# Kernel optimization log

Measured on AMD Instinct MI355X. Metric: run time of the kernel, lower is better.

Reference implementation:

```python
import jax, jax.numpy as jnp
import numpy as np

# ResNet-20 (CIFAR) conv shapes: conv1 + 18 block convs, all 3x3 pad=1
SHAPES = [(16,3,3,3)] + [(16,16,3,3)]*6 + [(32,16,3,3)] + [(32,32,3,3)]*5 + [(64,32,3,3)] + [(64,64,3,3)]*5
SIZES = [int(np.prod(s)) for s in SHAPES]
OFFS = np.concatenate([[0], np.cumsum(SIZES)]).astype(int)
D = int(OFFS[-1])  # 267696 flattened conv params
LOW_D = 40
# (conv_a, conv_b, stride, out_channels) for each BasicBlock
BLOCKS = [(1,2,1,16),(3,4,1,16),(5,6,1,16),
          (7,8,2,32),(9,10,1,32),(11,12,1,32),
          (13,14,2,64),(15,16,1,64),(17,18,1,64)]

def conv3x3(x, w, stride):
    return jax.lax.conv_general_dilated(x, w, (stride, stride), ((1,1),(1,1)),
        dimension_numbers=('NCHW','OIHW','NCHW'))

def bn(x):
    # training-mode BatchNorm2d with default-initialized affine (gamma=1, beta=0)
    m = jnp.mean(x, axis=(0,2,3), keepdims=True)
    v = jnp.var(x, axis=(0,2,3), keepdims=True)
    return (x - m) * jax.lax.rsqrt(v + 1e-5)

def shortcut(x, stride, out_ch):
    # option-A shortcut: stride-2 subsample + zero-pad channels
    if stride != 1:
        x = x[:, :, ::2, ::2]
    pad = out_ch - x.shape[1]
    if pad > 0:
        x = jnp.pad(x, ((0,0),(pad//2, pad - pad//2),(0,0),(0,0)))
    return x

def setup_inputs() -> dict:
    key = jax.random.key(0)
    ks = jax.random.split(key, 6)
    B = 1024
    x = jax.random.normal(ks[0], (B,3,32,32), jnp.float32)
    origin_weight = jax.random.normal(ks[1], (D,), jnp.float32) * 0.05
    P = jax.random.normal(ks[2], (LOW_D, D), jnp.float32) * 0.01
    new_param = jax.random.uniform(ks[3], (LOW_D,), jnp.float32)
    W_fc = jax.random.normal(ks[4], (10,64), jnp.float32) * 0.1
    b_fc = jnp.zeros((10,), jnp.float32)
    return {"x": x, "origin_weight": origin_weight, "P": P,
            "new_param": new_param, "W_fc": W_fc, "b_fc": b_fc}

def reference(x, origin_weight, P, new_param, W_fc, b_fc):
    # conv(x, W0) + sum_i a_i * conv(x, P_i)  ==  conv(x, W0 + sum_i a_i * P_i)
    # (conv is linear in its weights, so fusing the 40-term loop is exact)
    w_flat = origin_weight + new_param @ P  # [D]
    ws = [w_flat[OFFS[i]:OFFS[i+1]].reshape(SHAPES[i]) for i in range(19)]
    out = jax.nn.relu(bn(conv3x3(x, ws[0], 1)))
    for (a, b, s, c) in BLOCKS:
        h = jax.nn.relu(bn(conv3x3(out, ws[a], s)))
        h = bn(conv3x3(h, ws[b], 1))
        out = jax.nn.relu(h + shortcut(out, s, c))
    out = out.mean(axis=(2,3))  # global average pool -> [B, 64]
    return out @ W_fc.T + b_fc  # [B, 10]
```

## Files before the change

kernel.cpp:

```cpp
#include <hip/hip_runtime.h>
#include <hip/hip_bf16.h>

#define BATCH 1024
#define NLAYER 19
#define DTOT 267696
#define NSLOT 64
#define PSL (NSLOT*128)

typedef __attribute__((ext_vector_type(8))) short v8s;
typedef __attribute__((ext_vector_type(4))) float v4f;

__device__ inline float ldf(const float* p){ return *p; }
__device__ inline float ldf(const __hip_bfloat16* p){ return __bfloat162float(*p); }

__device__ inline unsigned short f2bf(float x){
    __hip_bfloat16 h = __float2bfloat16(x);
    return *reinterpret_cast<unsigned short*>(&h);
}
__device__ inline float bf2f(unsigned int u){
    return __uint_as_float(u << 16);
}

__global__ void detect_kernel(const unsigned short* __restrict__ xraw, int* __restrict__ flag)
{
    __shared__ int bad;
    if (threadIdx.x == 0) bad = 0;
    __syncthreads();
    int lbad = 0;
    for (int i = threadIdx.x; i < 4096; i += 256) {
        unsigned e = (xraw[i] >> 7) & 0xFF;
        if (e >= 147) lbad++;
    }
    if (lbad) atomicAdd(&bad, lbad);
    __syncthreads();
    if (threadIdx.x == 0) *flag = (bad == 0) ? 1 : 0;
}

__device__ inline bool flag_skip(const int* flag, int want)
{
    if (flag == nullptr) return false;
    return (*(volatile const int*)flag) != want;
}

template<typename T>
__global__ void wflat_kernel(const T* __restrict__ origin,
                             const T* __restrict__ P,
                             const T* __restrict__ npar,
                             float* __restrict__ wout, int D,
                             const int* flag, int want)
{
    if (flag_skip(flag, want)) return;
    int d = blockIdx.x*256 + threadIdx.x;
    if (d >= D) return;
    float acc = ldf(origin + d);
    #pragma unroll 8
    for (int k = 0; k < 40; k++)
        acc += ldf(npar + k) * ldf(P + (long long)k*D + d);
    wout[d] = acc;
}

__global__ void wprep_kernel(const float* __restrict__ wflat, unsigned short* __restrict__ WT)
{
    static const int CINA[19]  = {3,16,16,16,16,16,16,16,32,32,32,32,32,32,64,64,64,64,64};
    static const int COUTA[19] = {16,16,16,16,16,16,16,32,32,32,32,32,32,64,64,64,64,64,64};
    static const int LGCA[19]  = {0,4,4,4,4,4,4,4,5,5,5,5,5,5,6,6,6,6,6};
    static const int KPADA[19] = {0,160,160,160,160,160,160,160,288,288,288,288,288,288,576,576,576,576,576};
    static const int WOFFA[19] = {0,432,2736,5040,7344,9648,11952,14256,18864,
        28080,37296,46512,55728,64944,83376,120240,157104,193968,230832};
    static const int WTOFFA[19]= {0,0,2560,5120,7680,10240,12800,15360,20480,29696,
        38912,48128,57344,66560,84992,121856,158720,195584,232448};
    int l = blockIdx.z;
    if (l == 0) return;
    int co = blockIdx.y;
    if (co >= COUTA[l]) return;
    int kp = blockIdx.x*192 + threadIdx.x;
    if (kp >= KPADA[l]) return;
    int cin = CINA[l];
    float v = 0.f;
    if (kp < 9*cin) {
        int tap = kp >> LGCA[l];
        int ci  = kp & (cin - 1);
        v = wflat[WOFFA[l] + (co*cin + ci)*9 + tap];
    }
    WT[WTOFFA[l] + co*KPADA[l] + kp] = f2bf(v);
}

__device__ inline void ldpair(const float* base, int p, float& x0, float& x1){
    const float2 v = ((const float2*)base)[p];
    x0 = v.x; x1 = v.y;
}
__device__ inline void ldpair(const __hip_bfloat16* base, int p, float& x0, float& x1){
    unsigned u = ((const unsigned int*)base)[p];
    x0 = __uint_as_float(u << 16);
    x1 = __uint_as_float(u & 0xffff0000u);
}

template<typename T>
__global__ __launch_bounds__(512) void conv_l0(
    const T* __restrict__ in, const float* __restrict__ wt,
    unsigned short* __restrict__ out,
    const int* flag, int want)
{
    if (flag_skip(flag, want)) return;
    constexpr int WP = 38, W2 = 19;
    __shared__ uint2 smem2[2048];
    __shared__ unsigned int in_su[3*18*W2];

    const int tid  = threadIdx.x;
    const int b    = blockIdx.x >> 1;
    const int half = blockIdx.x & 1;
    const int row0 = half*16 - 1;

    {
        const T* inb = in + (size_t)b*3072;
        for (int i = tid; i < 864; i += 512) {
            int w2 = i & 15, lr = (i >> 4) % 18, c = i / 288;
            int ih = row0 + lr;
            unsigned int pk = 0u;
            if ((unsigned)ih < 32u) {
                float x0, x1;
                ldpair(inb, (c*32 + ih)*16 + w2, x0, x1);
                pk = (unsigned int)f2bf(x0) | ((unsigned int)f2bf(x1) << 16);
            }
            in_su[(c*18 + lr)*W2 + 1 + w2] = pk;
        }
        unsigned short* in_ss = (unsigned short*)in_su;
        for (int i = tid; i < 54; i += 512) {
            in_ss[i*WP + 1]  = 0;
            in_ss[i*WP + 34] = 0;
        }
    }
    __syncthreads();

    const int r   = tid >> 5;
    const int col = tid & 31;
    const bool odd = (col & 1);

    float xin[27];
    #pragma unroll
    for (int ci = 0; ci < 3; ci++) {
        #pragma unroll
        for (int kh = 0; kh < 3; kh++) {
            const unsigned int* up = in_su + (ci*18 + r + kh)*W2 + ((col+1) >> 1);
            unsigned int u0 = up[0], u1 = up[1];
            const int kb = ci*9 + kh*3;
            xin[kb+0] = odd ? bf2f(u0 & 0xffffu) : bf2f(u0 >> 16);
            xin[kb+1] = odd ? bf2f(u0 >> 16)     : bf2f(u1 & 0xffffu);
            xin[kb+2] = odd ? bf2f(u1 & 0xffffu) : bf2f(u1 >> 16);
        }
    }

    float acc[16];
    #pragma unroll
    for (int co = 0; co < 16; co++) {
        float a = 0.f;
        #pragma unroll
        for (int k = 0; k < 27; k++)
            a += xin[k] * wt[co*27 + k];
        acc[co] = a;
    }

    #pragma unroll
    for (int j = 0; j < 4; j++) {
        uint2 v;
        v.x = (unsigned)f2bf(acc[4*j+0]) | ((unsigned)f2bf(acc[4*j+1]) << 16);
        v.y = (unsigned)f2bf(acc[4*j+2]) | ((unsigned)f2bf(acc[4*j+3]) << 16);
        smem2[tid*4 + (j ^ (tid & 3))] = v;
    }
    __syncthreads();
    {
        uint2* ob = (uint2*)(out + (size_t)b*16384 + half*8192);
        #pragma unroll
        for (int it = 0; it < 4; it++) {
            int s = it*512 + tid;
            int phys = (s & ~3) | ((s & 3) ^ ((s >> 2) & 3));
            ob[s] = smem2[phys];
        }
    }
}

__global__ __launch_bounds__(256) void stats16_kernel(
    const unsigned short* __restrict__ x, float* __restrict__ ps, int n4)
{
    __shared__ float red[4][32];
    int t = blockIdx.x*256 + threadIdx.x;
    const int stride = gridDim.x*256;
    float s[4] = {0,0,0,0}, q[4] = {0,0,0,0};
    for (int i = t; i < n4; i += stride) {
        uint2 v = ((const uint2*)x)[i];
        float f0 = bf2f(v.x & 0xffffu), f1 = bf2f(v.x >> 16);
        float f2_ = bf2f(v.y & 0xffffu), f3 = bf2f(v.y >> 16);
        s[0] += f0; q[0] += f0*f0;
        s[1] += f1; q[1] += f1*f1;
        s[2] += f2_; q[2] += f2_*f2_;
        s[3] += f3; q[3] += f3*f3;
    }
    #pragma unroll
    for (int off = 4; off < 64; off <<= 1) {
        #pragma unroll
        for (int k = 0; k < 4; k++) {
            s[k] += __shfl_xor(s[k], off);
            q[k] += __shfl_xor(q[k], off);
        }
    }
    const int lane = threadIdx.x & 63, w = threadIdx.x >> 6;
    if (lane < 4) {
        #pragma unroll
        for (int k = 0; k < 4; k++) {
            red[w][lane*4 + k]      = s[k];
            red[w][16 + lane*4 + k] = q[k];
        }
    }
    __syncthreads();
    if (threadIdx.x < 32) {
        float v = red[0][threadIdx.x] + red[1][threadIdx.x]
                + red[2][threadIdx.x] + red[3][threadIdx.x];
        float* sl = ps + (blockIdx.x & (NSLOT-1))*128;
        atomicAdd(&sl[(threadIdx.x < 16) ? threadIdx.x : (48 + threadIdx.x)], v);
    }
}

template<int CIN, int COUT, int HIN, int WIN, int ST, bool FUSE, bool PN,
         bool FUSE2, int PREVC, int PADF>
__global__ __launch_bounds__(256, 4) void conv_mfma(
    const unsigned short* __restrict__ src, const unsigned short* __restrict__ prev,
    unsigned short* __restrict__ resid,
    const unsigned short* __restrict__ wt,
    unsigned short* __restrict__ out, float* __restrict__ stats,
    const float* __restrict__ nstats, float ninvN,
    const float* __restrict__ pstats, float pinvN)
{
    constexpr int HO = HIN/ST, WO = WIN/ST, M = HO*WO, MT = M/16;
    constexpr int NT = COUT/16;
    constexpr int K  = 9*CIN;
    constexpr int S  = (K + 31)/32;
    constexpr int KPAD = S*32;
    constexpr int lgC  = (CIN==16)?4:(CIN==32)?5:6;
    constexpr int lgWI = (WIN==32)?5:(WIN==16)?4:3;
    constexpr int lgWO = (WO==32)?5:(WO==16)?4:3;
    constexpr int CMASK = CIN/8 - 1;
    constexpr int JITER = (NT==1)? MT/4 : (NT==2)? MT/2 : MT;
    static_assert(M*COUT <= CIN*HIN*WIN, "out_s fits in in_s");

    __shared__ unsigned short in_s[CIN*HIN*WIN];
    __shared__ float red[128];
    __shared__ float statred[256];
    __shared__ float nm[64], nv[64];
    __shared__ float pm_s[64], pv_s[64];
    __shared__ uint4 zq;

    const int tid = threadIdx.x;
    const int b   = blockIdx.x;

    if (tid == 0) { zq.x = 0; zq.y = 0; zq.z = 0; zq.w = 0; }

    if (nstats != nullptr) {
        const int idx = tid & 127, hf = tid >> 7;
        float sacc = 0.f;
        #pragma unroll 8
        for (int k = hf*32; k < hf*32 + 32; k++)
            sacc += nstats[k*128 + idx];
        statred[tid] = sacc;
    }
    __syncthreads();
    if (nstats != nullptr && tid < CIN) {
        float ssum = statred[tid]      + statred[128 + tid];
        float qsum = statred[64 + tid] + statred[192 + tid];
        float m = ssum*ninvN;
        float v = fmaxf(qsum*ninvN - m*m, 0.f);
        nm[tid] = m; nv[tid] = rsqrtf(v + 1e-5f);
    }
    if (PN && tid < CIN) {
        float ssum = 0.f, qsum = 0.f;
        for (int k = 0; k < NSLOT; k++) {
            ssum += pstats[k*128 + tid];
            qsum += pstats[k*128 + 64 + tid];
        }
        float m = ssum*pinvN;
        float v = fmaxf(qsum*pinvN - m*m, 0.f);
        pm_s[tid] = m; pv_s[tid] = rsqrtf(v + 1e-5f);
    }
    __syncthreads();

    {
        const uint4* sb4 = (const uint4*)(src + (size_t)b*(HIN*WIN)*CIN);
        constexpr int NP4 = CIN*HIN*WIN/8;
        if (FUSE) {
            const uint4* pb4 = (const uint4*)(prev + (size_t)b*(HIN*WIN)*CIN);
            uint4* rb4 = (uint4*)(resid + (size_t)b*(HIN*WIN)*CIN);
            for (int i = tid; i < NP4; i += 256) {
                uint4 v = sb4[i];
                uint4 pw = pb4[i];
                int e0 = i << 3;
                int c0 = e0 & (CIN-1);
                int p  = e0 >> lgC;
                float f[8] = { bf2f(v.x & 0xffffu), bf2f(v.x >> 16),
                               bf2f(v.y & 0xffffu), bf2f(v.y >> 16),
                               bf2f(v.z & 0xffffu), bf2f(v.z >> 16),
                               bf2f(v.w & 0xffffu), bf2f(v.w >> 16) };
                float g[8] = { bf2f(pw.x & 0xffffu), bf2f(pw.x >> 16),
                               bf2f(pw.y & 0xffffu), bf2f(pw.y >> 16),
                               bf2f(pw.z & 0xffffu), bf2f(pw.z >> 16),
                               bf2f(pw.w & 0xffffu), bf2f(pw.w >> 16) };
                #pragma unroll
                for (int k = 0; k < 8; k++) {
                    int c = c0 + k;
                    float fx = (f[k] - nm[c])*nv[c];
                    float gv = g[k];
                    if (PN) gv = fmaxf((gv - pm_s[c])*pv_s[c], 0.f);
                    f[k] = fmaxf(fx + gv, 0.f);
                }
                uint4 o;
                o.x = (unsigned)f2bf(f[0]) | ((unsigned)f2bf(f[1]) << 16);
                o.y = (unsigned)f2bf(f[2]) | ((unsigned)f2bf(f[3]) << 16);
                o.z = (unsigned)f2bf(f[4]) | ((unsigned)f2bf(f[5]) << 16);
                o.w = (unsigned)f2bf(f[6]) | ((unsigned)f2bf(f[7]) << 16);
                rb4[i] = o;
                int csw = c0 ^ ((p & CMASK) << 3);
                *(uint4*)(in_s + (p << lgC) + csw) = o;
            }
        } else if (FUSE2) {
            uint4* rb4 = (uint4*)(resid + (size_t)b*(HIN*WIN)*CIN);
            for (int i = tid; i < NP4; i += 256) {
                uint4 v = sb4[i];
                int e0 = i << 3;
                int c0 = e0 & (CIN-1);
                int p  = e0 >> lgC;
                int h  = p >> lgWI, wq = p & (WIN-1);
                int pp = (h << (lgWI+2)) + 2*wq;
                int pc0 = c0 - PADF;
                bool pv = (pc0 >= 0) && (pc0 <= PREVC - 8);
                uint4 pw;
                pw.x = 0; pw.y = 0; pw.z = 0; pw.w = 0;
                if (pv) pw = *(const uint4*)(prev + ((size_t)b*(HIN*WIN*4) + pp)*PREVC + pc0);
                float f[8] = { bf2f(v.x & 0xffffu), bf2f(v.x >> 16),
                               bf2f(v.y & 0xffffu), bf2f(v.y >> 16),
                               bf2f(v.z & 0xffffu), bf2f(v.z >> 16),
                               bf2f(v.w & 0xffffu), bf2f(v.w >> 16) };
                float g[8] = { bf2f(pw.x & 0xffffu), bf2f(pw.x >> 16),
                               bf2f(pw.y & 0xffffu), bf2f(pw.y >> 16),
                               bf2f(pw.z & 0xffffu), bf2f(pw.z >> 16),
                               bf2f(pw.w & 0xffffu), bf2f(pw.w >> 16) };
                #pragma unroll
                for (int k = 0; k < 8; k++) {
                    int c = c0 + k;
                    f[k] = fmaxf((f[k] - nm[c])*nv[c] + g[k], 0.f);
                }
                uint4 o;
                o.x = (unsigned)f2bf(f[0]) | ((unsigned)f2bf(f[1]) << 16);
                o.y = (unsigned)f2bf(f[2]) | ((unsigned)f2bf(f[3]) << 16);
                o.z = (unsigned)f2bf(f[4]) | ((unsigned)f2bf(f[5]) << 16);
                o.w = (unsigned)f2bf(f[6]) | ((unsigned)f2bf(f[7]) << 16);
                rb4[i] = o;
                int csw = c0 ^ ((p & CMASK) << 3);
                *(uint4*)(in_s + (p << lgC) + csw) = o;
            }
        } else if (nstats == nullptr) {
            for (int i = tid; i < NP4; i += 256) {
                uint4 v = sb4[i];
                int e0 = i << 3;
                int c0 = e0 & (CIN-1);
                int p  = e0 >> lgC;
                int csw = c0 ^ ((p & CMASK) << 3);
                *(uint4*)(in_s + (p << lgC) + csw) = v;
            }
        } else {
            for (int i = tid; i < NP4; i += 256) {
                uint4 v = sb4[i];
                int e0 = i << 3;
                int c0 = e0 & (CIN-1);
                int p  = e0 >> lgC;
                float f[8] = { bf2f(v.x & 0xffffu), bf2f(v.x >> 16),
                               bf2f(v.y & 0xffffu), bf2f(v.y >> 16),
                               bf2f(v.z & 0xffffu), bf2f(v.z >> 16),
                               bf2f(v.w & 0xffffu), bf2f(v.w >> 16) };
                #pragma unroll
                for (int k = 0; k < 8; k++) {
                    int c = c0 + k;
                    f[k] = fmaxf((f[k] - nm[c])*nv[c], 0.f);
                }
                uint4 o;
                o.x = (unsigned)f2bf(f[0]) | ((unsigned)f2bf(f[1]) << 16);
                o.y = (unsigned)f2bf(f[2]) | ((unsigned)f2bf(f[3]) << 16);
                o.z = (unsigned)f2bf(f[4]) | ((unsigned)f2bf(f[5]) << 16);
                o.w = (unsigned)f2bf(f[6]) | ((unsigned)f2bf(f[7]) << 16);
                int csw = c0 ^ ((p & CMASK) << 3);
                *(uint4*)(in_s + (p << lgC) + csw) = o;
            }
        }
    }
    __syncthreads();

    const int w   = tid >> 6;
    const int ln  = tid & 63;
    const int l15 = ln & 15;
    const int q   = ln >> 4;

    int n0, mt0, step;
    if (NT == 1)      { n0 = 0;         mt0 = w;      step = 4; }
    else if (NT == 2) { n0 = (w&1)*16;  mt0 = w>>1;   step = 2; }
    else              { n0 = w*16;      mt0 = 0;      step = 1; }

    v8s Bf[S];
    {
        const unsigned short* wb = wt + (size_t)(n0 + l15)*KPAD + q*8;
        #pragma unroll
        for (int s = 0; s < S; s++)
            Bf[s] = *(const v8s*)(wb + 32*s);
    }

    int dh1s[S], dw1s[S];
    int c0q = (CIN==16) ? ((q & 1) << 3) : (q << 3);
    if (CIN == 16) {
        int tq = q >> 1;
        #pragma unroll
        for (int s = 0; s < S; s++) {
            int tap = 2*s + tq;
            int dh = (tap*11) >> 5;
            int dw = tap - 3*dh;
            dh1s[s] = (tap >= 9) ? -1000 : (dh - 1);
            dw1s[s] = dw - 1;
        }
    }

    v4f acc[JITER];
    #pragma unroll
    for (int j = 0; j < JITER; j++) acc[j] = v4f{0.f,0.f,0.f,0.f};

    #pragma unroll
    for (int j = 0; j < JITER; j++) {
        const int mt  = mt0 + j*step;
        const int p   = mt*16 + l15;
        const int ihb = (p >> lgWO) * ST;
        const int iwb = (p & (WO-1)) * ST;
        #pragma unroll
        for (int s = 0; s < S; s++) {
            int dh1, dw1, c0s;
            if (CIN == 16) { dh1 = dh1s[s]; dw1 = dw1s[s]; c0s = c0q; }
            else {
                const int tap = (CIN == 32) ? s : (s >> 1);
                dh1 = tap/3 - 1; dw1 = tap%3 - 1;
                c0s = c0q + ((CIN == 64) ? ((s & 1) << 5) : 0);
            }
            int ih = ihb + dh1, iw = iwb + dw1;
            bool valid = ((unsigned)ih < (unsigned)HIN) && ((unsigned)iw < (unsigned)WIN);
            int pp  = (ih << lgWI) + iw;
            int csw = c0s ^ ((pp & CMASK) << 3);
            int eoff = (pp << lgC) + csw;
            const v8s* ap = valid ? (const v8s*)(in_s + eoff) : (const v8s*)&zq;
            v8s Af = *ap;
            acc[j] = __builtin_amdgcn_mfma_f32_16x16x32_bf16(Af, Bf[s], acc[j], 0, 0, 0);
        }
    }
    __syncthreads();

    unsigned short* out_s = in_s;
    float sa = 0.f, qa = 0.f;
    #pragma unroll
    for (int j = 0; j < JITER; j++) {
        const int mt = mt0 + j*step;
        #pragma unroll
        for (int r2 = 0; r2 < 4; r2++) {
            float v = acc[j][r2];
            out_s[(mt*16 + q*4 + r2)*COUT + n0 + l15] = f2bf(v);
            sa += v; qa += v*v;
        }
    }
    __syncthreads();

    {
        constexpr int NIT = (M*COUT/8)/256;
        uint4* ob4 = (uint4*)(out + (size_t)b*M*COUT);
        const uint4* os4 = (const uint4*)in_s;
        #pragma unroll
        for (int it = 0; it < NIT; it++)
            ob4[it*256 + tid] = os4[it*256 + tid];
    }

    sa += __shfl_xor(sa, 16); sa += __shfl_xor(sa, 32);
    qa += __shfl_xor(qa, 16); qa += __shfl_xor(qa, 32);
    if (q == 0) {
        red[(w*16 + l15)*2]     = sa;
        red[(w*16 + l15)*2 + 1] = qa;
    }
    __syncthreads();
    if (tid < COUT) {
        float S2, Q2;
        if (NT == 1) {
            S2 = red[tid*2] + red[(16+tid)*2] + red[(32+tid)*2] + red[(48+tid)*2];
            Q2 = red[tid*2+1] + red[(16+tid)*2+1] + red[(32+tid)*2+1] + red[(48+tid)*2+1];
        } else if (NT == 2) {
            int w0 = tid >> 4, cl = tid & 15;
            S2 = red[((w0*16)+cl)*2]     + red[(((w0+2)*16)+cl)*2];
            Q2 = red[((w0*16)+cl)*2 + 1] + red[(((w0+2)*16)+cl)*2 + 1];
        } else {
            int w0 = tid >> 4, cl = tid & 15;
            S2 = red[((w0*16)+cl)*2];
            Q2 = red[((w0*16)+cl)*2 + 1];
        }
        float* sl = stats + (b & (NSLOT-1))*128;
        atomicAdd(&sl[tid],      S2);
        atomicAdd(&sl[64 + tid], Q2);
    }
}

__device__ inline void stf(float* p, float v){ *p = v; }
__device__ inline void stf(__hip_bfloat16* p, float v){ *p = __float2bfloat16(v); }

template<typename T>
__global__ void poolfc_kernel(const unsigned short* __restrict__ x,
    const unsigned short* __restrict__ resid,
    const float* __restrict__ stats, float invN,
    const T* __restrict__ Wfc, const T* __restrict__ bfc,
    T* __restrict__ out, const int* flag, int want)
{
    if (flag_skip(flag, want)) return;
    int b = blockIdx.x;
    int c = threadIdx.x;
    float ssum = 0.f, qsum = 0.f;
    for (int k = 0; k < NSLOT; k++) {
        ssum += stats[k*128 + c];
        qsum += stats[k*128 + 64 + c];
    }
    float m = ssum*invN;
    float v = fmaxf(qsum*invN - m*m, 0.f);
    float rs = rsqrtf(v + 1e-5f);
    float s = 0.f;
    #pragma unroll
    for (int p = 0; p < 64; p++) {
        size_t idx = ((size_t)b*64 + p)*64 + c;
        float xv = bf2f((unsigned int)x[idx]);
        float rv = bf2f((unsigned int)resid[idx]);
        s += fmaxf((xv - m)*rs + rv, 0.f);
    }
    __shared__ float feat[64];
    feat[c] = s * (1.f/64.f);
    __syncthreads();
    if (c < 10) {
        float o = ldf(bfc + c);
        for (int k = 0; k < 64; k++)
            o += feat[k] * ldf(Wfc + c*64 + k);
        stf(out + b*10 + c, o);
    }
}

extern "C" void kernel_launch(void* const* d_in, const int* in_sizes, int n_in,
                              void* d_out, int out_size, void* d_ws, size_t ws_size,
                              hipStream_t stream)
{
    char* ws = (char*)d_ws;
    float* wflat = (float*)(ws);
    int*   flag  = (int*)  (ws + 1146880);
    unsigned short* WT = (unsigned short*)(ws + 1179648);
    unsigned short* curA = (unsigned short*)(ws + 1720320);
    unsigned short* curB = (unsigned short*)(ws + 1720320 + 33554432ULL);
    unsigned short* f1   = (unsigned short*)(ws + 1720320 + 67108864ULL);
    unsigned short* f2   = (unsigned short*)(ws + 1720320 + 100663296ULL);
    float* ps    = (float*)(ws + 135938048ULL);

    hipMemsetAsync(ps, 0, NLAYER*PSL*4, stream);
    detect_kernel<<<1, 256, 0, stream>>>((const unsigned short*)d_in[0], flag);

    wflat_kernel<__hip_bfloat16><<<(DTOT+255)/256, 256, 0, stream>>>(
        (const __hip_bfloat16*)d_in[1], (const __hip_bfloat16*)d_in[2],
        (const __hip_bfloat16*)d_in[3], wflat, DTOT, flag, 1);
    wflat_kernel<float><<<(DTOT+255)/256, 256, 0, stream>>>(
        (const float*)d_in[1], (const float*)d_in[2],
        (const float*)d_in[3], wflat, DTOT, flag, 0);

    {
        dim3 g(3, 64, 19);
        wprep_kernel<<<g, 192, 0, stream>>>(wflat, WT);
    }

    static const int WTOFF[NLAYER] = {0,0,2560,5120,7680,10240,12800,15360,20480,29696,
        38912,48128,57344,66560,84992,121856,158720,195584,232448};
    const float iN32 = 1.f/1048576.f;
    const float iN16 = 1.f/262144.f;
    const float iN8  = 1.f/65536.f;

    conv_l0<__hip_bfloat16><<<2*BATCH,512,0,stream>>>(
        (const __hip_bfloat16*)d_in[0], wflat, curB, flag, 1);
    conv_l0<float><<<2*BATCH,512,0,stream>>>(
        (const float*)d_in[0], wflat, curB, flag, 0);
    stats16_kernel<<<512,256,0,stream>>>(curB, ps, 4194304);

    conv_mfma<16,16,32,32,1,false,false,false,0,0><<<BATCH,256,0,stream>>>(
        curB, nullptr, nullptr, WT + WTOFF[1], f1, ps + 1*PSL, ps, iN32, nullptr, 0.f);
    conv_mfma<16,16,32,32,1,false,false,false,0,0><<<BATCH,256,0,stream>>>(
        f1, nullptr, nullptr, WT + WTOFF[2], f2, ps + 2*PSL, ps + 1*PSL, iN32, nullptr, 0.f);
    conv_mfma<16,16,32,32,1,true,true,false,0,0><<<BATCH,256,0,stream>>>(
        f2, curB, curA, WT + WTOFF[3], f1, ps + 3*PSL, ps + 2*PSL, iN32, ps, iN32);
    conv_mfma<16,16,32,32,1,false,false,false,0,0><<<BATCH,256,0,stream>>>(
        f1, nullptr, nullptr, WT + WTOFF[4], f2, ps + 4*PSL, ps + 3*PSL, iN32, nullptr, 0.f);
    conv_mfma<16,16,32,32,1,true,false,false,0,0><<<BATCH,256,0,stream>>>(
        f2, curA, curB, WT + WTOFF[5], f1, ps + 5*PSL, ps + 4*PSL, iN32, nullptr, 0.f);
    conv_mfma<16,16,32,32,1,false,false,false,0,0><<<BATCH,256,0,stream>>>(
        f1, nullptr, nullptr, WT + WTOFF[6], f2, ps + 6*PSL, ps + 5*PSL, iN32, nullptr, 0.f);
    conv_mfma<16,32,32,32,2,true,false,false,0,0><<<BATCH,256,0,stream>>>(
        f2, curB, curA, WT + WTOFF[7], f1, ps + 7*PSL, ps + 6*PSL, iN32, nullptr, 0.f);
    conv_mfma<32,32,16,16,1,false,false,false,0,0><<<BATCH,256,0,stream>>>(
        f1, nullptr, nullptr, WT + WTOFF[8], f2, ps + 8*PSL, ps + 7*PSL, iN16, nullptr, 0.f);
    conv_mfma<32,32,16,16,1,false,false,true,16,8><<<BATCH,256,0,stream>>>(
        f2, curA, curB, WT + WTOFF[9], f1, ps + 9*PSL, ps + 8*PSL, iN16, nullptr, 0.f);
    conv_mfma<32,32,16,16,1,false,false,false,0,0><<<BATCH,256,0,stream>>>(
        f1, nullptr, nullptr, WT + WTOFF[10], f2, ps + 10*PSL, ps + 9*PSL, iN16, nullptr, 0.f);
    conv_mfma<32,32,16,16,1,true,false,false,0,0><<<BATCH,256,0,stream>>>(
        f2, curB, curA, WT + WTOFF[11], f1, ps + 11*PSL, ps + 10*PSL, iN16, nullptr, 0.f);
    conv_mfma<32,32,16,16,1,false,false,false,0,0><<<BATCH,256,0,stream>>>(
        f1, nullptr, nullptr, WT + WTOFF[12], f2, ps + 12*PSL, ps + 11*PSL, iN16, nullptr, 0.f);
    conv_mfma<32,64,16,16,2,true,false,false,0,0><<<BATCH,256,0,stream>>>(
        f2, curA, curB, WT + WTOFF[13], f1, ps + 13*PSL, ps + 12*PSL, iN16, nullptr, 0.f);
    conv_mfma<64,64,8,8,1,false,false,false,0,0><<<BATCH,256,0,stream>>>(
        f1, nullptr, nullptr, WT + WTOFF[14], f2, ps + 14*PSL, ps + 13*PSL, iN8, nullptr, 0.f);
    conv_mfma<64,64,8,8,1,false,false,true,32,16><<<BATCH,256,0,stream>>>(
        f2, curB, curA, WT + WTOFF[15], f1, ps + 15*PSL, ps + 14*PSL, iN8, nullptr, 0.f);
    conv_mfma<64,64,8,8,1,false,false,false,0,0><<<BATCH,256,0,stream>>>(
        f1, nullptr, nullptr, WT + WTOFF[16], f2, ps + 16*PSL, ps + 15*PSL, iN8, nullptr, 0.f);
    conv_mfma<64,64,8,8,1,true,false,false,0,0><<<BATCH,256,0,stream>>>(
        f2, curA, curB, WT + WTOFF[17], f1, ps + 17*PSL, ps + 16*PSL, iN8, nullptr, 0.f);
    conv_mfma<64,64,8,8,1,false,false,false,0,0><<<BATCH,256,0,stream>>>(
        f1, nullptr, nullptr, WT + WTOFF[18], f2, ps + 18*PSL, ps + 17*PSL, iN8, nullptr, 0.f);

    poolfc_kernel<__hip_bfloat16><<<BATCH, 64, 0, stream>>>(
        f2, curB, ps + 18*PSL, iN8,
        (const __hip_bfloat16*)d_in[4], (const __hip_bfloat16*)d_in[5],
        (__hip_bfloat16*)d_out, flag, 1);
    poolfc_kernel<float><<<BATCH, 64, 0, stream>>>(
        f2, curB, ps + 18*PSL, iN8,
        (const float*)d_in[4], (const float*)d_in[5],
        (float*)d_out, flag, 0);
}
```

Baseline: 471.5 us.

## Fuse layer-0 batchnorm statistics into conv_l0 and stream weights for CIN=64

The per-channel sum and sum-of-squares for the first conv output are now accumulated inside conv_l0 as it writes its tile, which removes the separate stats16_kernel pass that re-read the full activation tensor. For CIN=64 layers the MFMA loop order is swapped so each weight fragment is loaded inside the tap loop instead of holding all S fragments in registers. The aim is lower register pressure and better occupancy, at the cost of repeated weight loads from global/L1. The fused stats path adds 2048 atomics per launch into the same 64 slots.

Measured after the change: 459.2 us. 1.03x faster.

```diff
diff --git a/kernel.cpp b/kernel.cpp
--- a/kernel.cpp
+++ b/kernel.cpp
@@ -98,13 +98,14 @@
 template<typename T>
 __global__ __launch_bounds__(512) void conv_l0(
     const T* __restrict__ in, const float* __restrict__ wt,
-    unsigned short* __restrict__ out,
+    unsigned short* __restrict__ out, float* __restrict__ ps,
     const int* flag, int want)
 {
     if (flag_skip(flag, want)) return;
     constexpr int WP = 38, W2 = 19;
     __shared__ uint2 smem2[2048];
     __shared__ unsigned int in_su[3*18*W2];
+    __shared__ float sred[8][32];
 
     const int tid  = threadIdx.x;
     const int b    = blockIdx.x >> 1;
@@ -168,55 +169,49 @@
         smem2[tid*4 + (j ^ (tid & 3))] = v;
     }
     __syncthreads();
+
+    float s4[4] = {0,0,0,0}, q4[4] = {0,0,0,0};
     {
         uint2* ob = (uint2*)(out + (size_t)b*16384 + half*8192);
         #pragma unroll
         for (int it = 0; it < 4; it++) {
             int s = it*512 + tid;
             int phys = (s & ~3) | ((s & 3) ^ ((s >> 2) & 3));
-            ob[s] = smem2[phys];
-        }
-    }
-}
-
-__global__ __launch_bounds__(256) void stats16_kernel(
-    const unsigned short* __restrict__ x, float* __restrict__ ps, int n4)
-{
-    __shared__ float red[4][32];
-    int t = blockIdx.x*256 + threadIdx.x;
-    const int stride = gridDim.x*256;
-    float s[4] = {0,0,0,0}, q[4] = {0,0,0,0};
-    for (int i = t; i < n4; i += stride) {
-        uint2 v = ((const uint2*)x)[i];
-        float f0 = bf2f(v.x & 0xffffu), f1 = bf2f(v.x >> 16);
-        float f2_ = bf2f(v.y & 0xffffu), f3 = bf2f(v.y >> 16);
-        s[0] += f0; q[0] += f0*f0;
-        s[1] += f1; q[1] += f1*f1;
-        s[2] += f2_; q[2] += f2_*f2_;
-        s[3] += f3; q[3] += f3*f3;
+            uint2 v = smem2[phys];
+            ob[s] = v;
+            float f0 = bf2f(v.x & 0xffffu), f1v = bf2f(v.x >> 16);
+            float f2v = bf2f(v.y & 0xffffu), f3v = bf2f(v.y >> 16);
+            s4[0] += f0;  q4[0] += f0*f0;
+            s4[1] += f1v; q4[1] += f1v*f1v;
+            s4[2] += f2v; q4[2] += f2v*f2v;
+            s4[3] += f3v; q4[3] += f3v*f3v;
+        }
     }
     #pragma unroll
     for (int off = 4; off < 64; off <<= 1) {
         #pragma unroll
-        for (int k = 0; k < 4; k++) {
-            s[k] += __shfl_xor(s[k], off);
-            q[k] += __shfl_xor(q[k], off);
-        }
-    }
-    const int lane = threadIdx.x & 63, w = threadIdx.x >> 6;
-    if (lane < 4) {
-        #pragma unroll
-        for (int k = 0; k < 4; k++) {
-            red[w][lane*4 + k]      = s[k];
-            red[w][16 + lane*4 + k] = q[k];
-        }
-    }
-    __syncthreads();
-    if (threadIdx.x < 32) {
-        float v = red[0][threadIdx.x] + red[1][threadIdx.x]
-                + red[2][threadIdx.x] + red[3][threadIdx.x];
+        for (int k2 = 0; k2 < 4; k2++) {
+            s4[k2] += __shfl_xor(s4[k2], off);
+            q4[k2] += __shfl_xor(q4[k2], off);
+        }
+    }
+    {
+        const int lane = tid & 63, wv = tid >> 6;
+        if (lane < 4) {
+            #pragma unroll
+            for (int k2 = 0; k2 < 4; k2++) {
+                sred[wv][lane*4 + k2]      = s4[k2];
+                sred[wv][16 + lane*4 + k2] = q4[k2];
+            }
+        }
+    }
+    __syncthreads();
+    if (tid < 32) {
+        float a = 0.f;
+        #pragma unroll
+        for (int wv = 0; wv < 8; wv++) a += sred[wv][tid];
         float* sl = ps + (blockIdx.x & (NSLOT-1))*128;
-        atomicAdd(&sl[(threadIdx.x < 16) ? threadIdx.x : (48 + threadIdx.x)], v);
+        atomicAdd(&sl[(tid < 16) ? tid : (48 + tid)], a);
     }
 }
 
@@ -401,55 +396,75 @@
     else if (NT == 2) { n0 = (w&1)*16;  mt0 = w>>1;   step = 2; }
     else              { n0 = w*16;      mt0 = 0;      step = 1; }
 
-    v8s Bf[S];
-    {
-        const unsigned short* wb = wt + (size_t)(n0 + l15)*KPAD + q*8;
-        #pragma unroll
-        for (int s = 0; s < S; s++)
-            Bf[s] = *(const v8s*)(wb + 32*s);
-    }
-
-    int dh1s[S], dw1s[S];
-    int c0q = (CIN==16) ? ((q & 1) << 3) : (q << 3);
-    if (CIN == 16) {
-        int tq = q >> 1;
-        #pragma unroll
-        for (int s = 0; s < S; s++) {
-            int tap = 2*s + tq;
-            int dh = (tap*11) >> 5;
-            int dw = tap - 3*dh;
-            dh1s[s] = (tap >= 9) ? -1000 : (dh - 1);
-            dw1s[s] = dw - 1;
-        }
-    }
+    const unsigned short* wb = wt + (size_t)(n0 + l15)*KPAD + q*8;
+    const int c0q = (CIN==16) ? ((q & 1) << 3) : (q << 3);
 
     v4f acc[JITER];
     #pragma unroll
     for (int j = 0; j < JITER; j++) acc[j] = v4f{0.f,0.f,0.f,0.f};
 
-    #pragma unroll
-    for (int j = 0; j < JITER; j++) {
-        const int mt  = mt0 + j*step;
-        const int p   = mt*16 + l15;
-        const int ihb = (p >> lgWO) * ST;
-        const int iwb = (p & (WO-1)) * ST;
+    if constexpr (CIN == 64) {
         #pragma unroll
         for (int s = 0; s < S; s++) {
-            int dh1, dw1, c0s;
-            if (CIN == 16) { dh1 = dh1s[s]; dw1 = dw1s[s]; c0s = c0q; }
-            else {
-                const int tap = (CIN == 32) ? s : (s >> 1);
-                dh1 = tap/3 - 1; dw1 = tap%3 - 1;
-                c0s = c0q + ((CIN == 64) ? ((s & 1) << 5) : 0);
-            }
-            int ih = ihb + dh1, iw = iwb + dw1;
-            bool valid = ((unsigned)ih < (unsigned)HIN) && ((unsigned)iw < (unsigned)WIN);
-            int pp  = (ih << lgWI) + iw;
-            int csw = c0s ^ ((pp & CMASK) << 3);
-            int eoff = (pp << lgC) + csw;
-            const v8s* ap = valid ? (const v8s*)(in_s + eoff) : (const v8s*)&zq;
-            v8s Af = *ap;
-            acc[j] = __builtin_amdgcn_mfma_f32_16x16x32_bf16(Af, Bf[s], acc[j], 0, 0, 0);
+            const v8s Bf = *(const v8s*)(wb + 32*s);
+            const int tap = s >> 1;
+            const int dh1 = tap/3 - 1, dw1 = tap%3 - 1;
+            const int c0s = c0q + ((s & 1) << 5);
+            #pragma unroll
+            for (int j = 0; j < JITER; j++) {
+                const int mt  = mt0 + j*step;
+                const int p   = mt*16 + l15;
+                const int ihb = (p >> lgWO) * ST;
+                const int iwb = (p & (WO-1)) * ST;
+                int ih = ihb + dh1, iw = iwb + dw1;
+                bool valid = ((unsigned)ih < (unsigned)HIN) && ((unsigned)iw < (unsigned)WIN);
+                int pp  = (ih << lgWI) + iw;
+                int csw = c0s ^ ((pp & CMASK) << 3);
+                int eoff = (pp << lgC) + csw;
+                const v8s* ap = valid ? (const v8s*)(in_s + eoff) : (const v8s*)&zq;
+                v8s Af = *ap;
+                acc[j] = __builtin_amdgcn_mfma_f32_16x16x32_bf16(Af, Bf, acc[j], 0, 0, 0);
+            }
+        }
+    } else {
+        v8s Bf[S];
+        #pragma unroll
+        for (int s = 0; s < S; s++)
+            Bf[s] = *(const v8s*)(wb + 32*s);
+
+        int dh1s[S], dw1s[S];
+        if (CIN == 16) {
+            int tq = q >> 1;
+            #pragma unroll
+            for (int s = 0; s < S; s++) {
+                int tap = 2*s + tq;
+                int dh = (tap*11) >> 5;
+                int dw = tap - 3*dh;
+                dh1s[s] = (tap >= 9) ? -1000 : (dh - 1);
+                dw1s[s] = dw - 1;
+            }
+        }
+
+        #pragma unroll
+        for (int j = 0; j < JITER; j++) {
+            const int mt  = mt0 + j*step;
+            const int p   = mt*16 + l15;
+            const int ihb = (p >> lgWO) * ST;
+            const int iwb = (p & (WO-1)) * ST;
+            #pragma unroll
+            for (int s = 0; s < S; s++) {
+                int dh1, dw1;
+                if (CIN == 16) { dh1 = dh1s[s]; dw1 = dw1s[s]; }
+                else           { dh1 = s/3 - 1; dw1 = s%3 - 1; }
+                int ih = ihb + dh1, iw = iwb + dw1;
+                bool valid = ((unsigned)ih < (unsigned)HIN) && ((unsigned)iw < (unsigned)WIN);
+                int pp  = (ih << lgWI) + iw;
+                int csw = c0q ^ ((pp & CMASK) << 3);
+                int eoff = (pp << lgC) + csw;
+                const v8s* ap = valid ? (const v8s*)(in_s + eoff) : (const v8s*)&zq;
+                v8s Af = *ap;
+                acc[j] = __builtin_amdgcn_mfma_f32_16x16x32_bf16(Af, Bf[s], acc[j], 0, 0, 0);
+            }
         }
     }
     __syncthreads();
@@ -580,10 +595,9 @@
     const float iN8  = 1.f/65536.f;
 
     conv_l0<__hip_bfloat16><<<2*BATCH,512,0,stream>>>(
-        (const __hip_bfloat16*)d_in[0], wflat, curB, flag, 1);
+        (const __hip_bfloat16*)d_in[0], wflat, curB, ps, flag, 1);
     conv_l0<float><<<2*BATCH,512,0,stream>>>(
-        (const float*)d_in[0], wflat, curB, flag, 0);
-    stats16_kernel<<<512,256,0,stream>>>(curB, ps, 4194304);
+        (const float*)d_in[0], wflat, curB, ps, flag, 0);
 
     conv_mfma<16,16,32,32,1,false,false,false,0,0><<<BATCH,256,0,stream>>>(
         curB, nullptr, nullptr, WT + WTOFF[1], f1, ps + 1*PSL, ps, iN32, nullptr, 0.f);
```
